# Optimization experiments

Hardware: AMD Instinct MI355X
Metric: run time of the kernel (lower is better)

The kernel has to match this reference:

```python
import jax, jax.numpy as jnp
import numpy as np

H = 256   # node_hidden_dim == edge_hidden_dim

def _ln(x, g, b):
    m = x.mean(-1, keepdims=True)
    v = ((x - m) ** 2).mean(-1, keepdims=True)
    return (x - m) / jnp.sqrt(v + 1e-5) * g + b

def _slnn(x, W, b, g, beta):
    # Linear -> LayerNorm -> ReLU (SingleLayerNN)
    return jax.nn.relu(_ln(x @ W.T + b, g, beta))

def _gru_mean(x, Wih, Whh, bih, bhh):
    # x: [E, T, Din]; torch GRU gate order (r, z, n); returns mean over time of outputs [E, H]
    h0 = jnp.zeros((x.shape[0], Whh.shape[1]), x.dtype)
    def step(h, xt):
        gi = xt @ Wih.T + bih
        gh = h @ Whh.T + bhh
        ir, iz, inn = jnp.split(gi, 3, axis=-1)
        hr, hz, hn = jnp.split(gh, 3, axis=-1)
        r = jax.nn.sigmoid(ir + hr)
        z = jax.nn.sigmoid(iz + hz)
        n = jnp.tanh(inn + r * hn)
        h_new = (1.0 - z) * n + z * h
        return h_new, h_new
    _, ys = jax.lax.scan(step, h0, jnp.swapaxes(x, 0, 1))  # [T, E, H]
    return ys.mean(axis=0)

def setup_inputs() -> dict:
    key = jax.random.key(0)
    ks = iter(jax.random.split(key, 64))
    rn = lambda shape, s=1.0: (jax.random.normal(next(ks), shape, jnp.float32) * s)
    ru = lambda shape: jax.random.uniform(next(ks), shape, jnp.float32)
    ri = lambda shape, hi: jax.random.randint(next(ks), shape, 0, hi, jnp.int32)
    N0, N1, N2, E0, E1, T = 40000, 10000, 2000, 100000, 20000, 8
    Dn, De, FC, C = 128, 64, 512, 16
    inp = {
        'node_features': rn((N0, Dn)),
        'edge_features_0': rn((E0, T, De)),
        'edge_features_1': rn((E1, T, H)),
        'history_0': rn((N0, H)),
        'history_1': rn((N1, H)),
        'agg_history_1': rn((N2, H)),
        'subg_norm_1': ru((N1, 1)),
        'subg_norm_2': ru((N2, 1)),
        'norm_2': ru((N2, 1)),
        'src0': ri((E0,), N0), 'dst0': ri((E0,), N1),
        'src1': ri((E1,), N1), 'dst1': ri((E1,), N2),
        'self_nid0': ri((N1,), N0), 'self_nid1': ri((N2,), N1),
        # parameters
        'gru0_Wih': rn((3 * H, De), 0.05), 'gru0_Whh': rn((3 * H, H), 0.05),
        'gru0_bih': rn((3 * H,), 0.05), 'gru0_bhh': rn((3 * H,), 0.05),
        'gru1_Wih': rn((3 * H, H), 0.05), 'gru1_Whh': rn((3 * H, H), 0.05),
        'gru1_bih': rn((3 * H,), 0.05), 'gru1_bhh': rn((3 * H,), 0.05),
        'phi0_W': rn((H, Dn + H), 0.05), 'phi0_b': rn((H,), 0.05),
        'phi0_g': jnp.ones((H,)), 'phi0_beta': jnp.zeros((H,)),
        'phi1_W': rn((H, 2 * H), 0.05), 'phi1_b': rn((H,), 0.05),
        'phi1_g': jnp.ones((H,)), 'phi1_beta': jnp.zeros((H,)),
        'nu0_W': rn((H, 2 * H), 0.05), 'nu0_b': rn((H,), 0.05),
        'nu0_g': jnp.ones((H,)), 'nu0_beta': jnp.zeros((H,)),
        'nu1_W': rn((H, 2 * H), 0.05), 'nu1_b': rn((H,), 0.05),
        'nu1_g': jnp.ones((H,)), 'nu1_beta': jnp.zeros((H,)),
        'fc1_W': rn((FC, H), 0.05), 'fc1_b': rn((FC,), 0.05),
        'fc2_W': rn((C, FC), 0.05), 'fc2_b': rn((C,), 0.05),
    }
    return inp

def reference(node_features, edge_features_0, edge_features_1, history_0, history_1,
              agg_history_1, subg_norm_1, subg_norm_2, norm_2,
              gru0_Wih, gru0_Whh, gru0_bih, gru0_bhh,
              gru1_Wih, gru1_Whh, gru1_bih, gru1_bhh,
              phi0_W, phi0_b, phi0_g, phi0_beta,
              phi1_W, phi1_b, phi1_g, phi1_beta,
              nu0_W, nu0_b, nu0_g, nu0_beta,
              nu1_W, nu1_b, nu1_g, nu1_beta,
              fc1_W, fc1_b, fc2_W, fc2_b,
              src0, dst0, src1, dst1, self_nid0, self_nid1):
    N1, N2 = self_nid0.shape[0], self_nid1.shape[0]
    # ---- layer 0 ----
    self_h0 = _slnn(jnp.concatenate([jnp.zeros((N1, H), node_features.dtype),
                                     node_features[self_nid0]], 1),
                    phi0_W, phi0_b, phi0_g, phi0_beta)                       # [N1, H]
    edge_emb0 = _gru_mean(edge_features_0, gru0_Wih, gru0_Whh, gru0_bih, gru0_bhh)  # [E0, H]
    nb0 = _slnn(jnp.concatenate([node_features[src0], edge_emb0], 1),
                phi0_W, phi0_b, phi0_g, phi0_beta)
    msg0 = jax.nn.relu(nb0 - history_0[src0])
    delta_nb0 = jax.ops.segment_sum(msg0, dst0, num_segments=N1)             # scatter-sum
    new_h0 = (delta_nb0 - self_h0) * subg_norm_1
    h1 = _slnn(jnp.concatenate([new_h0, self_h0], 1), nu0_W, nu0_b, nu0_g, nu0_beta)  # [N1, H]
    # ---- layer 1 ----
    self_h1 = _slnn(jnp.concatenate([jnp.zeros((N2, H), h1.dtype), h1[self_nid1]], 1),
                    phi1_W, phi1_b, phi1_g, phi1_beta)                       # [N2, H]
    self_delta_h1 = self_h1 - history_1[self_nid1]
    edge_emb1 = _gru_mean(edge_features_1, gru1_Wih, gru1_Whh, gru1_bih, gru1_bhh)  # [E1, H]
    nb1 = _slnn(jnp.concatenate([h1[src1], edge_emb1], 1),
                phi1_W, phi1_b, phi1_g, phi1_beta)
    msg1 = jax.nn.relu(nb1 - history_1[src1])
    delta_nb1 = jax.ops.segment_sum(msg1, dst1, num_segments=N2)
    new_h1 = (delta_nb1 - self_delta_h1) * subg_norm_2 + agg_history_1 * norm_2
    h2 = _slnn(jnp.concatenate([new_h1, self_h1], 1), nu1_W, nu1_b, nu1_g, nu1_beta)  # [N2, H]
    # ---- readout (no activation between fc1 and fc2, as in source) ----
    logit = (h2 @ fc1_W.T + fc1_b) @ fc2_W.T + fc2_b
    return logit
```

## Files before the change

### kernel.cpp

```cpp
#include <hip/hip_runtime.h>

typedef unsigned short u16;
typedef __attribute__((ext_vector_type(4))) float f32x4;
typedef __attribute__((ext_vector_type(8))) short bf16x8;
#define MFMA16(a,b,c) __builtin_amdgcn_mfma_f32_16x16x32_bf16((a),(b),(c),0,0,0)

__device__ __forceinline__ u16 f2bf(float f){
  unsigned int u = __float_as_uint(f);
  u += 0x7FFFu + ((u >> 16) & 1u);
  return (u16)(u >> 16);
}
__device__ __forceinline__ float bf2f(u16 h){
  return __uint_as_float(((unsigned int)h) << 16);
}
__device__ __forceinline__ float sigmoid_f(float x){
  x = fminf(fmaxf(x, -30.f), 30.f);
  return __fdividef(1.f, 1.f + __expf(-x));
}
__device__ __forceinline__ float tanh_f(float x){
  x = fminf(fmaxf(x, -15.f), 15.f);
  float e = __expf(-2.f * x);
  return __fdividef(1.f - e, 1.f + e);
}

__global__ void cvt_bf16_kernel(const float* __restrict__ in, u16* __restrict__ out, int n){
  int i = blockIdx.x * 256 + threadIdx.x;
  int stride = gridDim.x * 256;
  for (; i < n; i += stride) out[i] = f2bf(in[i]);
}

template<int R>
__device__ __forceinline__ void ln_stats_rows(const float* __restrict__ O,
                                              float* __restrict__ mean_s,
                                              float* __restrict__ rstd_s){
  const int tid  = threadIdx.x;
  const int wave = tid >> 6, lane = tid & 63;
  constexpr int RW = R / 4;
  #pragma unroll
  for (int rr = 0; rr < RW; rr++){
    const int r = wave * RW + rr;
    float s = 0.f, q = 0.f;
    #pragma unroll
    for (int i = lane; i < 256; i += 64){ float v = O[r*256 + i]; s += v; q += v*v; }
    #pragma unroll
    for (int off = 32; off; off >>= 1){ s += __shfl_down(s, off); q += __shfl_down(q, off); }
    if (lane == 0){
      float m   = s * (1.f/256.f);
      float var = q * (1.f/256.f) - m*m;
      mean_s[r] = m;
      rstd_s[r] = rsqrtf(fmaxf(var, 0.f) + 1e-5f);
    }
  }
}

template<int DIN, int NFD>
__global__ __launch_bounds__(256, 2)
void gru_mfma_kernel(int E,
    const float* __restrict__ x,
    const float* __restrict__ nodef,
    const int*   __restrict__ src,
    const int*   __restrict__ dst,
    const float* __restrict__ hist,
    const u16*   __restrict__ Wih,
    const u16*   __restrict__ Whh,
    const float* __restrict__ bih,
    const float* __restrict__ bhh,
    const u16*   __restrict__ phiW,
    const float* __restrict__ phib,
    const float* __restrict__ phig,
    const float* __restrict__ phibeta,
    float* __restrict__ delta)
{
  constexpr int HP  = 264;
  constexpr int XW  = (DIN > NFD) ? DIN : NFD;
  constexpr int XLP = XW + 8;
  constexpr int KP  = NFD + 256;

  __shared__ u16  hb[2 * 32 * HP];
  __shared__ u16  xl[32 * XLP];
  __shared__ float sums_s[4 * 32], sqs_s[4 * 32];
  __shared__ float mean_s[32], rstd_s[32];
  __shared__ int   srcs_s[32], dsts_s[32];

  const int tid  = threadIdx.x;
  const int wave = tid >> 6, lane = tid & 63;
  const int quad = lane >> 4, ln15 = lane & 15;
  const int cbase = wave * 64;
  const int e0   = blockIdx.x * 32;

  if (tid < 32){
    int e = e0 + tid;
    int ec = (e < E) ? e : (E - 1);
    srcs_s[tid] = src[ec];
    dsts_s[tid] = dst[ec];
  }

  int cnt[4];
  float brc[4], bzc[4], bnic[4], bnhc[4], pb[4], gg[4], gb[4];
  #pragma unroll
  for (int nt = 0; nt < 4; nt++){
    int c = cbase + nt*16 + ln15;
    cnt[nt]  = c;
    brc[nt]  = bih[c]       + bhh[c];
    bzc[nt]  = bih[256 + c] + bhh[256 + c];
    bnic[nt] = bih[512 + c];
    bnhc[nt] = bhh[512 + c];
    pb[nt]   = phib[c];
    gg[nt]   = phig[c];
    gb[nt]   = phibeta[c];
  }

  const int aoff = ln15 * HP  + quad * 8;
  const int xoff = ln15 * XLP + quad * 8;
  const int qoff = quad * 8;

  float hs[2][4][4];
  #pragma unroll
  for (int mt = 0; mt < 2; mt++)
    #pragma unroll
    for (int nt = 0; nt < 4; nt++)
      #pragma unroll
      for (int q = 0; q < 4; q++) hs[mt][nt][q] = 0.f;

  const f32x4 zero4 = {0.f, 0.f, 0.f, 0.f};

  for (int t = 0; t < 8; t++){
    __syncthreads();
    {
      constexpr int R4 = DIN / 4;
      for (int i = tid; i < 32 * R4; i += 256){
        int e  = i / R4;
        int k4 = (i - e * R4) * 4;
        int ge = (e0 + e < E) ? (e0 + e) : (E - 1);
        const float4 v = *(const float4*)(x + (size_t)ge * (8 * DIN) + (size_t)t * DIN + k4);
        ushort4 u;
        u.x = f2bf(v.x); u.y = f2bf(v.y); u.z = f2bf(v.z); u.w = f2bf(v.w);
        *(ushort4*)(xl + e * XLP + k4) = u;
      }
    }
    __syncthreads();

    const u16* rd = hb + ((t & 1) ^ 1) * (32 * HP);
    u16*       wr = hb + (t & 1) * (32 * HP);

    #pragma unroll 1
    for (int half = 0; half < 2; half++){
      f32x4 aR[2][2], aZ[2][2], aNI[2][2], aNH[2][2];
      #pragma unroll
      for (int mt = 0; mt < 2; mt++)
        #pragma unroll
        for (int j = 0; j < 2; j++){
          aR[mt][j] = zero4; aZ[mt][j] = zero4; aNI[mt][j] = zero4; aNH[mt][j] = zero4;
        }

      if (t > 0){
        #pragma unroll
        for (int kt = 0; kt < 8; kt++){
          bf16x8 a0 = *(const bf16x8*)(rd + aoff + kt * 32);
          bf16x8 a1 = *(const bf16x8*)(rd + aoff + 16 * HP + kt * 32);
          #pragma unroll
          for (int j = 0; j < 2; j++){
            const int nt = half * 2 + j;
            const u16* bp = Whh + (size_t)cnt[nt] * 256 + kt * 32 + qoff;
            bf16x8 br = *(const bf16x8*)(bp);
            bf16x8 bz = *(const bf16x8*)(bp + 256 * 256);
            bf16x8 bn = *(const bf16x8*)(bp + 512 * 256);
            aR[0][j]  = MFMA16(a0, br, aR[0][j]);  aR[1][j]  = MFMA16(a1, br, aR[1][j]);
            aZ[0][j]  = MFMA16(a0, bz, aZ[0][j]);  aZ[1][j]  = MFMA16(a1, bz, aZ[1][j]);
            aNH[0][j] = MFMA16(a0, bn, aNH[0][j]); aNH[1][j] = MFMA16(a1, bn, aNH[1][j]);
          }
        }
      }
      #pragma unroll
      for (int kt = 0; kt < DIN / 32; kt++){
        bf16x8 a0 = *(const bf16x8*)(xl + xoff + kt * 32);
        bf16x8 a1 = *(const bf16x8*)(xl + xoff + 16 * XLP + kt * 32);
        #pragma unroll
        for (int j = 0; j < 2; j++){
          const int nt = half * 2 + j;
          const u16* bp = Wih + (size_t)cnt[nt] * DIN + kt * 32 + qoff;
          bf16x8 br = *(const bf16x8*)(bp);
          bf16x8 bz = *(const bf16x8*)(bp + 256 * DIN);
          bf16x8 bn = *(const bf16x8*)(bp + 512 * DIN);
          aR[0][j]  = MFMA16(a0, br, aR[0][j]);  aR[1][j]  = MFMA16(a1, br, aR[1][j]);
          aZ[0][j]  = MFMA16(a0, bz, aZ[0][j]);  aZ[1][j]  = MFMA16(a1, bz, aZ[1][j]);
          aNI[0][j] = MFMA16(a0, bn, aNI[0][j]); aNI[1][j] = MFMA16(a1, bn, aNI[1][j]);
        }
      }
      #pragma unroll
      for (int mt = 0; mt < 2; mt++)
        #pragma unroll
        for (int j = 0; j < 2; j++){
          const int nt = half * 2 + j;
          const int c  = cnt[nt];
          #pragma unroll
          for (int q = 0; q < 4; q++){
            const int e = mt * 16 + quad * 4 + q;
            float r = sigmoid_f(aR[mt][j][q] + brc[nt]);
            float z = sigmoid_f(aZ[mt][j][q] + bzc[nt]);
            float n = tanh_f(aNI[mt][j][q] + bnic[nt] + r * (aNH[mt][j][q] + bnhc[nt]));
            float hold = (t > 0) ? bf2f(rd[e * HP + c]) : 0.f;
            float hnew = (1.f - z) * n + z * hold;
            hs[mt][nt][q] += hnew;
            if (t < 7) wr[e * HP + c] = f2bf(hnew);
          }
        }
    }
  }

  __syncthreads();
  {
    u16* eb = hb;
    #pragma unroll
    for (int mt = 0; mt < 2; mt++)
      #pragma unroll
      for (int nt = 0; nt < 4; nt++)
        #pragma unroll
        for (int q = 0; q < 4; q++){
          const int e = mt * 16 + quad * 4 + q;
          eb[e * HP + cnt[nt]] = f2bf(hs[mt][nt][q] * 0.125f);
        }
    constexpr int R4 = NFD / 4;
    for (int i = tid; i < 32 * R4; i += 256){
      int e  = i / R4;
      int k4 = (i - e * R4) * 4;
      const float4 v = *(const float4*)(nodef + (size_t)srcs_s[e] * NFD + k4);
      ushort4 u;
      u.x = f2bf(v.x); u.y = f2bf(v.y); u.z = f2bf(v.z); u.w = f2bf(v.w);
      *(ushort4*)(xl + e * XLP + k4) = u;
    }
  }
  __syncthreads();

  f32x4 P[2][4];
  #pragma unroll
  for (int mt = 0; mt < 2; mt++)
    #pragma unroll
    for (int nt = 0; nt < 4; nt++) P[mt][nt] = zero4;

  #pragma unroll
  for (int kt = 0; kt < NFD / 32; kt++){
    bf16x8 a0 = *(const bf16x8*)(xl + xoff + kt * 32);
    bf16x8 a1 = *(const bf16x8*)(xl + xoff + 16 * XLP + kt * 32);
    #pragma unroll
    for (int nt = 0; nt < 4; nt++){
      const u16* bp = phiW + (size_t)cnt[nt] * KP + kt * 32 + qoff;
      bf16x8 b = *(const bf16x8*)(bp);
      P[0][nt] = MFMA16(a0, b, P[0][nt]);
      P[1][nt] = MFMA16(a1, b, P[1][nt]);
    }
  }
  #pragma unroll
  for (int kt = 0; kt < 8; kt++){
    bf16x8 a0 = *(const bf16x8*)(hb + aoff + kt * 32);
    bf16x8 a1 = *(const bf16x8*)(hb + aoff + 16 * HP + kt * 32);
    #pragma unroll
    for (int nt = 0; nt < 4; nt++){
      const u16* bp = phiW + (size_t)cnt[nt] * KP + NFD + kt * 32 + qoff;
      bf16x8 b = *(const bf16x8*)(bp);
      P[0][nt] = MFMA16(a0, b, P[0][nt]);
      P[1][nt] = MFMA16(a1, b, P[1][nt]);
    }
  }

  float sl[2][4], sq[2][4];
  #pragma unroll
  for (int mt = 0; mt < 2; mt++)
    #pragma unroll
    for (int q = 0; q < 4; q++){ sl[mt][q] = 0.f; sq[mt][q] = 0.f; }
  #pragma unroll
  for (int mt = 0; mt < 2; mt++)
    #pragma unroll
    for (int nt = 0; nt < 4; nt++)
      #pragma unroll
      for (int q = 0; q < 4; q++){
        float v = P[mt][nt][q] + pb[nt];
        P[mt][nt][q] = v;
        sl[mt][q] += v;
        sq[mt][q] += v * v;
      }
  #pragma unroll
  for (int off = 1; off < 16; off <<= 1){
    #pragma unroll
    for (int mt = 0; mt < 2; mt++)
      #pragma unroll
      for (int q = 0; q < 4; q++){
        sl[mt][q] += __shfl_xor(sl[mt][q], off);
        sq[mt][q] += __shfl_xor(sq[mt][q], off);
      }
  }
  if (ln15 == 0){
    #pragma unroll
    for (int mt = 0; mt < 2; mt++)
      #pragma unroll
      for (int q = 0; q < 4; q++){
        int row = mt * 16 + quad * 4 + q;
        sums_s[wave * 32 + row] = sl[mt][q];
        sqs_s[wave * 32 + row]  = sq[mt][q];
      }
  }
  __syncthreads();
  if (tid < 32){
    float m = 0.f, qq = 0.f;
    #pragma unroll
    for (int w = 0; w < 4; w++){ m += sums_s[w * 32 + tid]; qq += sqs_s[w * 32 + tid]; }
    m  *= (1.f / 256.f);
    qq *= (1.f / 256.f);
    mean_s[tid] = m;
    rstd_s[tid] = rsqrtf(fmaxf(qq - m * m, 0.f) + 1e-5f);
  }
  __syncthreads();

  #pragma unroll
  for (int mt = 0; mt < 2; mt++)
    #pragma unroll
    for (int nt = 0; nt < 4; nt++){
      const int c = cnt[nt];
      #pragma unroll
      for (int q = 0; q < 4; q++){
        const int e  = mt * 16 + quad * 4 + q;
        const int ge = e0 + e;
        float y = (P[mt][nt][q] - mean_s[e]) * rstd_s[e] * gg[nt] + gb[nt];
        y = fmaxf(y, 0.f);
        float mv = y - hist[(size_t)srcs_s[e] * 256 + c];
        if (ge < E && mv > 0.f)
          atomicAdd(delta + (size_t)dsts_s[e] * 256 + c, mv);
      }
    }
}

template<int K, int WS>
__global__ __launch_bounds__(256)
void self_slnn_kernel(int N,
    const float* __restrict__ feat,
    const int*   __restrict__ nid,
    const float* __restrict__ W,
    const float* __restrict__ b,
    const float* __restrict__ g,
    const float* __restrict__ beta,
    const float* __restrict__ hist,
    float* __restrict__ out,
    float* __restrict__ out2)
{
  constexpr int R = 8;
  __shared__ float X[R*K];
  __shared__ float O[R*256];
  __shared__ float mean_s[R], rstd_s[R];
  __shared__ int   nids[R];
  const int tid = threadIdx.x;
  const int n0  = blockIdx.x * R;
  if (tid < R) nids[tid] = (n0 + tid < N) ? nid[n0 + tid] : 0;
  __syncthreads();
  for (int i = tid; i < R*K; i += 256){
    int r = i / K, k = i - r*K;
    X[i] = feat[(size_t)nids[r]*K + k];
  }
  __syncthreads();
  const int c = tid;
  const float* Wc = W + (size_t)c*WS + (WS - K);
  float acc[R];
  const float bc0 = b[c];
  #pragma unroll
  for (int r = 0; r < R; r++) acc[r] = bc0;
  #pragma unroll 1
  for (int k = 0; k < K; k += 4){
    float4 w = *(const float4*)(Wc + k);
    #pragma unroll
    for (int r = 0; r < R; r++){
      float4 xv = *(const float4*)(X + r*K + k);
      acc[r] += w.x*xv.x + w.y*xv.y + w.z*xv.z + w.w*xv.w;
    }
  }
  #pragma unroll
  for (int r = 0; r < R; r++) O[r*256 + c] = acc[r];
  __syncthreads();
  ln_stats_rows<R>(O, mean_s, rstd_s);
  __syncthreads();
  const float gc = g[c], bc = beta[c];
  #pragma unroll
  for (int r = 0; r < R; r++){
    int n = n0 + r;
    if (n < N){
      float y = fmaxf((acc[r] - mean_s[r]) * rstd_s[r] * gc + bc, 0.f);
      out[(size_t)n*256 + c] = y;
      if (out2) out2[(size_t)n*256 + c] = y - hist[(size_t)nids[r]*256 + c];
    }
  }
}

__global__ __launch_bounds__(256)
void compose_slnn_kernel(int N,
    const float* __restrict__ delta,
    const float* __restrict__ selfA,
    const float* __restrict__ selfB,
    const float* __restrict__ subg,
    const float* __restrict__ agg,
    const float* __restrict__ normv,
    const float* __restrict__ W,
    const float* __restrict__ b,
    const float* __restrict__ g,
    const float* __restrict__ beta,
    float* __restrict__ out)
{
  constexpr int R = 8;
  __shared__ float X[R*512];
  __shared__ float O[R*256];
  __shared__ float mean_s[R], rstd_s[R];
  const int tid = threadIdx.x;
  const int n0  = blockIdx.x * R;
  for (int i = tid; i < R*512; i += 256){
    int r = i >> 9, k = i & 511;
    int n = n0 + r;
    float v = 0.f;
    if (n < N){
      if (k < 256){
        v = (delta[(size_t)n*256 + k] - selfA[(size_t)n*256 + k]) * subg[n];
        if (agg) v += agg[(size_t)n*256 + k] * normv[n];
      } else {
        v = selfB[(size_t)n*256 + (k - 256)];
      }
    }
    X[i] = v;
  }
  __syncthreads();
  const int c = tid;
  const float* Wc = W + (size_t)c*512;
  float acc[R];
  const float bc0 = b[c];
  #pragma unroll
  for (int r = 0; r < R; r++) acc[r] = bc0;
  #pragma unroll 1
  for (int k = 0; k < 512; k += 4){
    float4 w = *(const float4*)(Wc + k);
    #pragma unroll
    for (int r = 0; r < R; r++){
      float4 xv = *(const float4*)(X + r*512 + k);
      acc[r] += w.x*xv.x + w.y*xv.y + w.z*xv.z + w.w*xv.w;
    }
  }
  #pragma unroll
  for (int r = 0; r < R; r++) O[r*256 + c] = acc[r];
  __syncthreads();
  ln_stats_rows<R>(O, mean_s, rstd_s);
  __syncthreads();
  const float gc = g[c], bc = beta[c];
  #pragma unroll
  for (int r = 0; r < R; r++){
    int n = n0 + r;
    if (n < N)
      out[(size_t)n*256 + c] = fmaxf((acc[r] - mean_s[r]) * rstd_s[r] * gc + bc, 0.f);
  }
}

__global__ __launch_bounds__(256)
void readout_kernel(int N,
    const float* __restrict__ h2,
    const float* __restrict__ W1,
    const float* __restrict__ b1,
    const float* __restrict__ W2,
    const float* __restrict__ b2,
    float* __restrict__ out)
{
  constexpr int R = 8;
  __shared__ float X[R*256];
  __shared__ float T[R*512];
  const int tid = threadIdx.x;
  const int n0  = blockIdx.x * R;
  for (int i = tid; i < R*256; i += 256){
    int r = i >> 8, k = i & 255;
    int n = n0 + r;
    X[i] = (n < N) ? h2[(size_t)n*256 + k] : 0.f;
  }
  __syncthreads();
  const int c = tid;
  const float* Wa = W1 + (size_t)c*256;
  const float* Wb = W1 + (size_t)(c+256)*256;
  float acca[R], accb[R];
  const float ba = b1[c], bb = b1[c+256];
  #pragma unroll
  for (int r = 0; r < R; r++){ acca[r] = ba; accb[r] = bb; }
  #pragma unroll 1
  for (int k = 0; k < 256; k += 4){
    float4 wa = *(const float4*)(Wa + k);
    float4 wb = *(const float4*)(Wb + k);
    #pragma unroll
    for (int r = 0; r < R; r++){
      float4 xv = *(const float4*)(X + r*256 + k);
      acca[r] += wa.x*xv.x + wa.y*xv.y + wa.z*xv.z + wa.w*xv.w;
      accb[r] += wb.x*xv.x + wb.y*xv.y + wb.z*xv.z + wb.w*xv.w;
    }
  }
  #pragma unroll
  for (int r = 0; r < R; r++){ T[r*512 + c] = acca[r]; T[r*512 + 256 + c] = accb[r]; }
  __syncthreads();
  if (tid < R*16){
    int r = tid >> 4, o = tid & 15;
    int n = n0 + r;
    if (n < N){
      float s = b2[o];
      const float* w  = W2 + (size_t)o*512;
      const float* tr = T + r*512;
      #pragma unroll 4
      for (int k = 0; k < 512; k++) s += tr[k]*w[k];
      out[(size_t)n*16 + o] = s;
    }
  }
}

extern "C" void kernel_launch(void* const* d_in, const int* in_sizes, int n_in,
                              void* d_out, int out_size, void* d_ws, size_t ws_size,
                              hipStream_t stream) {
  const float* nf     = (const float*)d_in[0];
  const float* x0     = (const float*)d_in[1];
  const float* x1     = (const float*)d_in[2];
  const float* hist0  = (const float*)d_in[3];
  const float* hist1  = (const float*)d_in[4];
  const float* aggh1  = (const float*)d_in[5];
  const float* subg1  = (const float*)d_in[6];
  const float* subg2  = (const float*)d_in[7];
  const float* norm2  = (const float*)d_in[8];
  const int*   src0   = (const int*)d_in[9];
  const int*   dst0   = (const int*)d_in[10];
  const int*   src1   = (const int*)d_in[11];
  const int*   dst1   = (const int*)d_in[12];
  const int*   nid0   = (const int*)d_in[13];
  const int*   nid1   = (const int*)d_in[14];
  const float* g0Wih  = (const float*)d_in[15];
  const float* g0Whh  = (const float*)d_in[16];
  const float* g0bih  = (const float*)d_in[17];
  const float* g0bhh  = (const float*)d_in[18];
  const float* g1Wih  = (const float*)d_in[19];
  const float* g1Whh  = (const float*)d_in[20];
  const float* g1bih  = (const float*)d_in[21];
  const float* g1bhh  = (const float*)d_in[22];
  const float* phi0W  = (const float*)d_in[23];
  const float* phi0b  = (const float*)d_in[24];
  const float* phi0g  = (const float*)d_in[25];
  const float* phi0be = (const float*)d_in[26];
  const float* phi1W  = (const float*)d_in[27];
  const float* phi1b  = (const float*)d_in[28];
  const float* phi1g  = (const float*)d_in[29];
  const float* phi1be = (const float*)d_in[30];
  const float* nu0W   = (const float*)d_in[31];
  const float* nu0b   = (const float*)d_in[32];
  const float* nu0g   = (const float*)d_in[33];
  const float* nu0be  = (const float*)d_in[34];
  const float* nu1W   = (const float*)d_in[35];
  const float* nu1b   = (const float*)d_in[36];
  const float* nu1g   = (const float*)d_in[37];
  const float* nu1be  = (const float*)d_in[38];
  const float* fc1W   = (const float*)d_in[39];
  const float* fc1b   = (const float*)d_in[40];
  const float* fc2W   = (const float*)d_in[41];
  const float* fc2b   = (const float*)d_in[42];

  const int E0 = in_sizes[9];
  const int E1 = in_sizes[11];
  const int N1 = in_sizes[13];
  const int N2 = in_sizes[14];

  float* ws     = (float*)d_ws;
  float* delta0 = ws;
  float* selfh0 = delta0 + (size_t)N1*256;
  float* h1p    = selfh0 + (size_t)N1*256;
  float* delta1 = h1p    + (size_t)N1*256;
  float* selfh1 = delta1 + (size_t)N2*256;
  float* selfd1 = selfh1 + (size_t)N2*256;
  float* h2p    = selfd1 + (size_t)N2*256;

  u16* wbf       = (u16*)(h2p + (size_t)N2*256);
  u16* g0Wih_bf  = wbf;
  u16* g0Whh_bf  = g0Wih_bf + 768*64;
  u16* phi0W_bf  = g0Whh_bf + 768*256;
  u16* g1Wih_bf  = phi0W_bf + 256*384;
  u16* g1Whh_bf  = g1Wih_bf + 768*256;
  u16* phi1W_bf  = g1Whh_bf + 768*256;

  hipMemsetAsync(delta0, 0, (size_t)N1*256*sizeof(float), stream);
  hipMemsetAsync(delta1, 0, (size_t)N2*256*sizeof(float), stream);

  cvt_bf16_kernel<<<192, 256, 0, stream>>>(g0Wih, g0Wih_bf, 768*64);
  cvt_bf16_kernel<<<768, 256, 0, stream>>>(g0Whh, g0Whh_bf, 768*256);
  cvt_bf16_kernel<<<384, 256, 0, stream>>>(phi0W, phi0W_bf, 256*384);
  cvt_bf16_kernel<<<768, 256, 0, stream>>>(g1Wih, g1Wih_bf, 768*256);
  cvt_bf16_kernel<<<768, 256, 0, stream>>>(g1Whh, g1Whh_bf, 768*256);
  cvt_bf16_kernel<<<512, 256, 0, stream>>>(phi1W, phi1W_bf, 256*512);

  const int gN1 = (N1 + 7) / 8;
  const int gN2 = (N2 + 7) / 8;

  self_slnn_kernel<128, 384><<<gN1, 256, 0, stream>>>(
      N1, nf, nid0, phi0W, phi0b, phi0g, phi0be, nullptr, selfh0, nullptr);

  gru_mfma_kernel<64, 128><<<(E0 + 31) / 32, 256, 0, stream>>>(
      E0, x0, nf, src0, dst0, hist0,
      g0Wih_bf, g0Whh_bf, g0bih, g0bhh,
      phi0W_bf, phi0b, phi0g, phi0be, delta0);

  compose_slnn_kernel<<<gN1, 256, 0, stream>>>(
      N1, delta0, selfh0, selfh0, subg1, nullptr, nullptr,
      nu0W, nu0b, nu0g, nu0be, h1p);

  self_slnn_kernel<256, 512><<<gN2, 256, 0, stream>>>(
      N2, h1p, nid1, phi1W, phi1b, phi1g, phi1be, hist1, selfh1, selfd1);

  gru_mfma_kernel<256, 256><<<(E1 + 31) / 32, 256, 0, stream>>>(
      E1, x1, h1p, src1, dst1, hist1,
      g1Wih_bf, g1Whh_bf, g1bih, g1bhh,
      phi1W_bf, phi1b, phi1g, phi1be, delta1);

  compose_slnn_kernel<<<gN2, 256, 0, stream>>>(
      N2, delta1, selfd1, selfh1, subg2, aggh1, norm2,
      nu1W, nu1b, nu1g, nu1be, h2p);

  readout_kernel<<<gN2, 256, 0, stream>>>(
      N2, h2p, fc1W, fc1b, fc2W, fc2b, (float*)d_out);

  (void)n_in; (void)out_size; (void)ws_size;
}
```

Baseline: 3.263 ms.

## Restructure GRU MFMA kernel with larger edge tiles, chunked LDS layout, register prefetch

Rewrites the fused GRU+phi kernel to take a templated edge tile (64 for layer 0), so each Whh/Wih fragment loaded from global feeds more MFMAs. Shared memory moves to a k-chunk-major layout without padding, the previous hidden state stays packed in registers, and the next timestep's input is prefetched into registers during compute. It also folds biases into the accumulator init, uses faster exp2/rcp sigmoid/tanh without clamping, and uses packed bf16 conversion. In exchange, register pressure and LDS use rise, which may cut occupancy, and the approximate activations can change accuracy slightly.

```diff
diff --git a/kernel.cpp b/kernel.cpp
--- a/kernel.cpp
+++ b/kernel.cpp
@@ -13,6 +13,30 @@
 __device__ __forceinline__ float bf2f(u16 h){
   return __uint_as_float(((unsigned int)h) << 16);
 }
+
+#if defined(__has_builtin)
+#  if __has_builtin(__builtin_amdgcn_cvt_pk_bf16_f32)
+#    define PK_BF16 1
+#  endif
+#endif
+__device__ __forceinline__ unsigned int pack_bf(float a, float b){
+#ifdef PK_BF16
+  auto v = __builtin_amdgcn_cvt_pk_bf16_f32(a, b);
+  return __builtin_bit_cast(unsigned int, v);
+#else
+  return (unsigned int)f2bf(a) | ((unsigned int)f2bf(b) << 16);
+#endif
+}
+
+__device__ __forceinline__ float fsig(float x){
+  float e = __builtin_amdgcn_exp2f(-1.44269504f * x);
+  return __builtin_amdgcn_rcpf(1.f + e);
+}
+__device__ __forceinline__ float ftanh(float x){
+  float e = __builtin_amdgcn_exp2f(2.88539008f * x);
+  return 1.f - 2.f * __builtin_amdgcn_rcpf(1.f + e);
+}
+
 __device__ __forceinline__ float sigmoid_f(float x){
   x = fminf(fmaxf(x, -30.f), 30.f);
   return __fdividef(1.f, 1.f + __expf(-x));
@@ -53,9 +77,9 @@
   }
 }
 
-template<int DIN, int NFD>
+template<int TM, int DIN, int NFD>
 __global__ __launch_bounds__(256, 2)
-void gru_mfma_kernel(int E,
+void gru_mfma2_kernel(int E,
     const float* __restrict__ x,
     const float* __restrict__ nodef,
     const int*   __restrict__ src,
@@ -71,218 +95,249 @@
     const float* __restrict__ phibeta,
     float* __restrict__ delta)
 {
-  constexpr int HP  = 264;
-  constexpr int XW  = (DIN > NFD) ? DIN : NFD;
-  constexpr int XLP = XW + 8;
-  constexpr int KP  = NFD + 256;
-
-  __shared__ u16  hb[2 * 32 * HP];
-  __shared__ u16  xl[32 * XLP];
-  __shared__ float sums_s[4 * 32], sqs_s[4 * 32];
-  __shared__ float mean_s[32], rstd_s[32];
-  __shared__ int   srcs_s[32], dsts_s[32];
+  constexpr int MT = TM / 16;
+  constexpr int KP = NFD + 256;
+  constexpr int HB = TM * 256;
+
+  __shared__ u16  hb[2 * HB];
+  __shared__ u16  xl[TM * DIN];
+  __shared__ float sums_s[4 * TM], sqs_s[4 * TM];
+  __shared__ float mean_s[TM], rstd_s[TM];
+  __shared__ int   srcs_s[TM], dsts_s[TM];
 
   const int tid  = threadIdx.x;
   const int wave = tid >> 6, lane = tid & 63;
   const int quad = lane >> 4, ln15 = lane & 15;
   const int cbase = wave * 64;
-  const int e0   = blockIdx.x * 32;
-
-  if (tid < 32){
+  const int e0   = blockIdx.x * TM;
+
+  if (tid < TM){
     int e = e0 + tid;
     int ec = (e < E) ? e : (E - 1);
     srcs_s[tid] = src[ec];
     dsts_s[tid] = dst[ec];
   }
 
-  int cnt[4];
-  float brc[4], bzc[4], bnic[4], bnhc[4], pb[4], gg[4], gb[4];
+  float brc[4], bzc[4], bnic[4], bnhc[4];
   #pragma unroll
   for (int nt = 0; nt < 4; nt++){
-    int c = cbase + nt*16 + ln15;
-    cnt[nt]  = c;
+    int c = cbase + nt * 16 + ln15;
     brc[nt]  = bih[c]       + bhh[c];
     bzc[nt]  = bih[256 + c] + bhh[256 + c];
     bnic[nt] = bih[512 + c];
     bnhc[nt] = bhh[512 + c];
-    pb[nt]   = phib[c];
-    gg[nt]   = phig[c];
-    gb[nt]   = phibeta[c];
-  }
-
-  const int aoff = ln15 * HP  + quad * 8;
-  const int xoff = ln15 * XLP + quad * 8;
+  }
+
   const int qoff = quad * 8;
 
-  float hs[2][4][4];
-  #pragma unroll
-  for (int mt = 0; mt < 2; mt++)
-    #pragma unroll
-    for (int nt = 0; nt < 4; nt++)
-      #pragma unroll
-      for (int q = 0; q < 4; q++) hs[mt][nt][q] = 0.f;
-
-  const f32x4 zero4 = {0.f, 0.f, 0.f, 0.f};
-
+  constexpr int TPR = 256 / TM;
+  constexpr int CPT = DIN / TPR;
+  const int srow   = tid / TPR;
+  const int schunk = (tid - srow * TPR) * CPT;
+  const float* xrowp = x + (size_t)((e0 + srow < E) ? (e0 + srow) : (E - 1)) * (8 * DIN) + schunk;
+
+  float4 xr[CPT / 4];
+  #pragma unroll
+  for (int i = 0; i < CPT / 4; i++) xr[i] = *(const float4*)(xrowp + i * 4);
+
+  f32x4 hs[4][MT];
+  unsigned int hprev[4][MT][2];
+  #pragma unroll
+  for (int nt = 0; nt < 4; nt++)
+    #pragma unroll
+    for (int mt = 0; mt < MT; mt++){
+      hs[nt][mt] = (f32x4){0.f,0.f,0.f,0.f};
+      hprev[nt][mt][0] = 0u; hprev[nt][mt][1] = 0u;
+    }
+
+  #pragma unroll 1
   for (int t = 0; t < 8; t++){
     __syncthreads();
-    {
-      constexpr int R4 = DIN / 4;
-      for (int i = tid; i < 32 * R4; i += 256){
-        int e  = i / R4;
-        int k4 = (i - e * R4) * 4;
-        int ge = (e0 + e < E) ? (e0 + e) : (E - 1);
-        const float4 v = *(const float4*)(x + (size_t)ge * (8 * DIN) + (size_t)t * DIN + k4);
-        ushort4 u;
-        u.x = f2bf(v.x); u.y = f2bf(v.y); u.z = f2bf(v.z); u.w = f2bf(v.w);
-        *(ushort4*)(xl + e * XLP + k4) = u;
-      }
+    #pragma unroll
+    for (int i = 0; i < CPT / 8; i++){
+      uint4 w;
+      w.x = pack_bf(xr[2*i].x,   xr[2*i].y);
+      w.y = pack_bf(xr[2*i].z,   xr[2*i].w);
+      w.z = pack_bf(xr[2*i+1].x, xr[2*i+1].y);
+      w.w = pack_bf(xr[2*i+1].z, xr[2*i+1].w);
+      *(uint4*)(xl + ((schunk/8 + i) * TM + srow) * 8) = w;
     }
     __syncthreads();
 
-    const u16* rd = hb + ((t & 1) ^ 1) * (32 * HP);
-    u16*       wr = hb + (t & 1) * (32 * HP);
-
-    #pragma unroll 1
-    for (int half = 0; half < 2; half++){
-      f32x4 aR[2][2], aZ[2][2], aNI[2][2], aNH[2][2];
-      #pragma unroll
-      for (int mt = 0; mt < 2; mt++)
-        #pragma unroll
-        for (int j = 0; j < 2; j++){
-          aR[mt][j] = zero4; aZ[mt][j] = zero4; aNI[mt][j] = zero4; aNH[mt][j] = zero4;
-        }
+    const u16* rd = hb + ((t + 1) & 1) * HB;
+    u16*       wr = hb + (t & 1) * HB;
+
+    #pragma unroll
+    for (int nt = 0; nt < 4; nt++){
+      const int c = cbase + nt * 16 + ln15;
+      f32x4 aR  = {brc[nt],  brc[nt],  brc[nt],  brc[nt]};
+      f32x4 aZ  = {bzc[nt],  bzc[nt],  bzc[nt],  bzc[nt]};
+      f32x4 aNI = {bnic[nt], bnic[nt], bnic[nt], bnic[nt]};
+      f32x4 aNH = {bnhc[nt], bnhc[nt], bnhc[nt], bnhc[nt]};
+      f32x4 accR[MT], accZ[MT], accNI[MT], accNH[MT];
+      #pragma unroll
+      for (int mt = 0; mt < MT; mt++){ accR[mt]=aR; accZ[mt]=aZ; accNI[mt]=aNI; accNH[mt]=aNH; }
 
       if (t > 0){
         #pragma unroll
         for (int kt = 0; kt < 8; kt++){
-          bf16x8 a0 = *(const bf16x8*)(rd + aoff + kt * 32);
-          bf16x8 a1 = *(const bf16x8*)(rd + aoff + 16 * HP + kt * 32);
+          bf16x8 a[MT];
           #pragma unroll
-          for (int j = 0; j < 2; j++){
-            const int nt = half * 2 + j;
-            const u16* bp = Whh + (size_t)cnt[nt] * 256 + kt * 32 + qoff;
-            bf16x8 br = *(const bf16x8*)(bp);
-            bf16x8 bz = *(const bf16x8*)(bp + 256 * 256);
-            bf16x8 bn = *(const bf16x8*)(bp + 512 * 256);
-            aR[0][j]  = MFMA16(a0, br, aR[0][j]);  aR[1][j]  = MFMA16(a1, br, aR[1][j]);
-            aZ[0][j]  = MFMA16(a0, bz, aZ[0][j]);  aZ[1][j]  = MFMA16(a1, bz, aZ[1][j]);
-            aNH[0][j] = MFMA16(a0, bn, aNH[0][j]); aNH[1][j] = MFMA16(a1, bn, aNH[1][j]);
+          for (int mt = 0; mt < MT; mt++)
+            a[mt] = *(const bf16x8*)(rd + ((kt*4 + quad) * TM + mt*16 + ln15) * 8);
+          const u16* bp = Whh + (size_t)c * 256 + kt * 32 + qoff;
+          bf16x8 br = *(const bf16x8*)(bp);
+          bf16x8 bz = *(const bf16x8*)(bp + 256 * 256);
+          bf16x8 bn = *(const bf16x8*)(bp + 512 * 256);
+          #pragma unroll
+          for (int mt = 0; mt < MT; mt++){
+            accR[mt]  = MFMA16(a[mt], br, accR[mt]);
+            accZ[mt]  = MFMA16(a[mt], bz, accZ[mt]);
+            accNH[mt] = MFMA16(a[mt], bn, accNH[mt]);
           }
         }
       }
       #pragma unroll
       for (int kt = 0; kt < DIN / 32; kt++){
-        bf16x8 a0 = *(const bf16x8*)(xl + xoff + kt * 32);
-        bf16x8 a1 = *(const bf16x8*)(xl + xoff + 16 * XLP + kt * 32);
+        bf16x8 a[MT];
         #pragma unroll
-        for (int j = 0; j < 2; j++){
-          const int nt = half * 2 + j;
-          const u16* bp = Wih + (size_t)cnt[nt] * DIN + kt * 32 + qoff;
-          bf16x8 br = *(const bf16x8*)(bp);
-          bf16x8 bz = *(const bf16x8*)(bp + 256 * DIN);
-          bf16x8 bn = *(const bf16x8*)(bp + 512 * DIN);
-          aR[0][j]  = MFMA16(a0, br, aR[0][j]);  aR[1][j]  = MFMA16(a1, br, aR[1][j]);
-          aZ[0][j]  = MFMA16(a0, bz, aZ[0][j]);  aZ[1][j]  = MFMA16(a1, bz, aZ[1][j]);
-          aNI[0][j] = MFMA16(a0, bn, aNI[0][j]); aNI[1][j] = MFMA16(a1, bn, aNI[1][j]);
+        for (int mt = 0; mt < MT; mt++)
+          a[mt] = *(const bf16x8*)(xl + ((kt*4 + quad) * TM + mt*16 + ln15) * 8);
+        const u16* up = Wih + (size_t)c * DIN + kt * 32 + qoff;
+        bf16x8 ur = *(const bf16x8*)(up);
+        bf16x8 uz = *(const bf16x8*)(up + 256 * DIN);
+        bf16x8 un = *(const bf16x8*)(up + 512 * DIN);
+        #pragma unroll
+        for (int mt = 0; mt < MT; mt++){
+          accR[mt]  = MFMA16(a[mt], ur, accR[mt]);
+          accZ[mt]  = MFMA16(a[mt], uz, accZ[mt]);
+          accNI[mt] = MFMA16(a[mt], un, accNI[mt]);
         }
       }
-      #pragma unroll
-      for (int mt = 0; mt < 2; mt++)
+
+      #pragma unroll
+      for (int mt = 0; mt < MT; mt++){
+        const int wbase = ((c >> 3) * TM + mt*16 + quad*4) * 8 + (c & 7);
         #pragma unroll
-        for (int j = 0; j < 2; j++){
-          const int nt = half * 2 + j;
-          const int c  = cnt[nt];
-          #pragma unroll
-          for (int q = 0; q < 4; q++){
-            const int e = mt * 16 + quad * 4 + q;
-            float r = sigmoid_f(aR[mt][j][q] + brc[nt]);
-            float z = sigmoid_f(aZ[mt][j][q] + bzc[nt]);
-            float n = tanh_f(aNI[mt][j][q] + bnic[nt] + r * (aNH[mt][j][q] + bnhc[nt]));
-            float hold = (t > 0) ? bf2f(rd[e * HP + c]) : 0.f;
-            float hnew = (1.f - z) * n + z * hold;
-            hs[mt][nt][q] += hnew;
-            if (t < 7) wr[e * HP + c] = f2bf(hnew);
+        for (int p = 0; p < 2; p++){
+          float h0 = bf2f((u16)(hprev[nt][mt][p]));
+          float h1 = bf2f((u16)(hprev[nt][mt][p] >> 16));
+          float r0 = fsig(accR[mt][2*p]),   r1 = fsig(accR[mt][2*p+1]);
+          float z0 = fsig(accZ[mt][2*p]),   z1 = fsig(accZ[mt][2*p+1]);
+          float n0 = ftanh(accNI[mt][2*p]   + r0 * accNH[mt][2*p]);
+          float n1 = ftanh(accNI[mt][2*p+1] + r1 * accNH[mt][2*p+1]);
+          float hn0 = n0 + z0 * (h0 - n0);
+          float hn1 = n1 + z1 * (h1 - n1);
+          hs[nt][mt][2*p]   += hn0;
+          hs[nt][mt][2*p+1] += hn1;
+          unsigned int pk = pack_bf(hn0, hn1);
+          hprev[nt][mt][p] = pk;
+          if (t < 7){
+            wr[wbase + (2*p)   * 8] = (u16)pk;
+            wr[wbase + (2*p+1) * 8] = (u16)(pk >> 16);
           }
         }
-    }
-  }
-
-  __syncthreads();
+      }
+      asm volatile("" ::: "memory");
+    }
+
+    if (t < 7){
+      const float* xp = xrowp + (t + 1) * DIN;
+      #pragma unroll
+      for (int i = 0; i < CPT / 4; i++) xr[i] = *(const float4*)(xp + i * 4);
+    }
+  }
+
+  __syncthreads();
+
   {
     u16* eb = hb;
     #pragma unroll
-    for (int mt = 0; mt < 2; mt++)
-      #pragma unroll
-      for (int nt = 0; nt < 4; nt++)
+    for (int nt = 0; nt < 4; nt++){
+      const int c = cbase + nt * 16 + ln15;
+      #pragma unroll
+      for (int mt = 0; mt < MT; mt++){
+        const int base = ((c >> 3) * TM + mt*16 + quad*4) * 8 + (c & 7);
         #pragma unroll
-        for (int q = 0; q < 4; q++){
-          const int e = mt * 16 + quad * 4 + q;
-          eb[e * HP + cnt[nt]] = f2bf(hs[mt][nt][q] * 0.125f);
-        }
-    constexpr int R4 = NFD / 4;
-    for (int i = tid; i < 32 * R4; i += 256){
-      int e  = i / R4;
-      int k4 = (i - e * R4) * 4;
-      const float4 v = *(const float4*)(nodef + (size_t)srcs_s[e] * NFD + k4);
-      ushort4 u;
-      u.x = f2bf(v.x); u.y = f2bf(v.y); u.z = f2bf(v.z); u.w = f2bf(v.w);
-      *(ushort4*)(xl + e * XLP + k4) = u;
-    }
-  }
-  __syncthreads();
-
-  f32x4 P[2][4];
-  #pragma unroll
-  for (int mt = 0; mt < 2; mt++)
-    #pragma unroll
-    for (int nt = 0; nt < 4; nt++) P[mt][nt] = zero4;
-
-  #pragma unroll
-  for (int kt = 0; kt < NFD / 32; kt++){
-    bf16x8 a0 = *(const bf16x8*)(xl + xoff + kt * 32);
-    bf16x8 a1 = *(const bf16x8*)(xl + xoff + 16 * XLP + kt * 32);
-    #pragma unroll
-    for (int nt = 0; nt < 4; nt++){
-      const u16* bp = phiW + (size_t)cnt[nt] * KP + kt * 32 + qoff;
-      bf16x8 b = *(const bf16x8*)(bp);
-      P[0][nt] = MFMA16(a0, b, P[0][nt]);
-      P[1][nt] = MFMA16(a1, b, P[1][nt]);
-    }
-  }
-  #pragma unroll
-  for (int kt = 0; kt < 8; kt++){
-    bf16x8 a0 = *(const bf16x8*)(hb + aoff + kt * 32);
-    bf16x8 a1 = *(const bf16x8*)(hb + aoff + 16 * HP + kt * 32);
-    #pragma unroll
-    for (int nt = 0; nt < 4; nt++){
-      const u16* bp = phiW + (size_t)cnt[nt] * KP + NFD + kt * 32 + qoff;
-      bf16x8 b = *(const bf16x8*)(bp);
-      P[0][nt] = MFMA16(a0, b, P[0][nt]);
-      P[1][nt] = MFMA16(a1, b, P[1][nt]);
-    }
-  }
-
-  float sl[2][4], sq[2][4];
-  #pragma unroll
-  for (int mt = 0; mt < 2; mt++)
+        for (int q = 0; q < 4; q++)
+          eb[base + q * 8] = f2bf(hs[nt][mt][q] * 0.125f);
+      }
+    }
+    u16* nb = hb + HB;
+    constexpr int NCPT = NFD / TPR;
+    const int nrow   = tid / TPR;
+    const int nchunk = (tid - nrow * TPR) * NCPT;
+    const float* np = nodef + (size_t)srcs_s[nrow] * NFD + nchunk;
+    #pragma unroll
+    for (int i = 0; i < NCPT / 8; i++){
+      float4 va = *(const float4*)(np + i * 8);
+      float4 vb = *(const float4*)(np + i * 8 + 4);
+      uint4 w;
+      w.x = pack_bf(va.x, va.y); w.y = pack_bf(va.z, va.w);
+      w.z = pack_bf(vb.x, vb.y); w.w = pack_bf(vb.z, vb.w);
+      *(uint4*)(nb + ((nchunk/8 + i) * TM + nrow) * 8) = w;
+    }
+  }
+  __syncthreads();
+
+  float pb[4], gg[4], gb[4];
+  #pragma unroll
+  for (int nt = 0; nt < 4; nt++){
+    int c = cbase + nt * 16 + ln15;
+    pb[nt] = phib[c]; gg[nt] = phig[c]; gb[nt] = phibeta[c];
+  }
+
+  f32x4 P[4][MT];
+  #pragma unroll
+  for (int nt = 0; nt < 4; nt++)
+    #pragma unroll
+    for (int mt = 0; mt < MT; mt++)
+      P[nt][mt] = (f32x4){pb[nt], pb[nt], pb[nt], pb[nt]};
+
+  #pragma unroll
+  for (int nt = 0; nt < 4; nt++){
+    const int c = cbase + nt * 16 + ln15;
+    #pragma unroll
+    for (int kt = 0; kt < NFD / 32; kt++){
+      bf16x8 a[MT];
+      #pragma unroll
+      for (int mt = 0; mt < MT; mt++)
+        a[mt] = *(const bf16x8*)(hb + HB + ((kt*4 + quad) * TM + mt*16 + ln15) * 8);
+      bf16x8 b = *(const bf16x8*)(phiW + (size_t)c * KP + kt * 32 + qoff);
+      #pragma unroll
+      for (int mt = 0; mt < MT; mt++) P[nt][mt] = MFMA16(a[mt], b, P[nt][mt]);
+    }
+    #pragma unroll
+    for (int kt = 0; kt < 8; kt++){
+      bf16x8 a[MT];
+      #pragma unroll
+      for (int mt = 0; mt < MT; mt++)
+        a[mt] = *(const bf16x8*)(hb + ((kt*4 + quad) * TM + mt*16 + ln15) * 8);
+      bf16x8 b = *(const bf16x8*)(phiW + (size_t)c * KP + NFD + kt * 32 + qoff);
+      #pragma unroll
+      for (int mt = 0; mt < MT; mt++) P[nt][mt] = MFMA16(a[mt], b, P[nt][mt]);
+    }
+    asm volatile("" ::: "memory");
+  }
+
+  float sl[MT][4], sq[MT][4];
+  #pragma unroll
+  for (int mt = 0; mt < MT; mt++)
     #pragma unroll
     for (int q = 0; q < 4; q++){ sl[mt][q] = 0.f; sq[mt][q] = 0.f; }
   #pragma unroll
-  for (int mt = 0; mt < 2; mt++)
-    #pragma unroll
-    for (int nt = 0; nt < 4; nt++)
+  for (int nt = 0; nt < 4; nt++)
+    #pragma unroll
+    for (int mt = 0; mt < MT; mt++)
       #pragma unroll
       for (int q = 0; q < 4; q++){
-        float v = P[mt][nt][q] + pb[nt];
-        P[mt][nt][q] = v;
-        sl[mt][q] += v;
-        sq[mt][q] += v * v;
+        float v = P[nt][mt][q];
+        sl[mt][q] += v; sq[mt][q] += v * v;
       }
   #pragma unroll
   for (int off = 1; off < 16; off <<= 1){
     #pragma unroll
-    for (int mt = 0; mt < 2; mt++)
+    for (int mt = 0; mt < MT; mt++)
       #pragma unroll
       for (int q = 0; q < 4; q++){
         sl[mt][q] += __shfl_xor(sl[mt][q], off);
@@ -291,19 +346,19 @@
   }
   if (ln15 == 0){
     #pragma unroll
-    for (int mt = 0; mt < 2; mt++)
+    for (int mt = 0; mt < MT; mt++)
       #pragma unroll
       for (int q = 0; q < 4; q++){
-        int row = mt * 16 + quad * 4 + q;
-        sums_s[wave * 32 + row] = sl[mt][q];
-        sqs_s[wave * 32 + row]  = sq[mt][q];
-      }
-  }
-  __syncthreads();
-  if (tid < 32){
+        int row = mt*16 + quad*4 + q;
+        sums_s[wave * TM + row] = sl[mt][q];
+        sqs_s[wave * TM + row]  = sq[mt][q];
+      }
+  }
+  __syncthreads();
+  if (tid < TM){
     float m = 0.f, qq = 0.f;
     #pragma unroll
-    for (int w = 0; w < 4; w++){ m += sums_s[w * 32 + tid]; qq += sqs_s[w * 32 + tid]; }
+    for (int w = 0; w < 4; w++){ m += sums_s[w * TM + tid]; qq += sqs_s[w * TM + tid]; }
     m  *= (1.f / 256.f);
     qq *= (1.f / 256.f);
     mean_s[tid] = m;
@@ -312,21 +367,22 @@
   __syncthreads();
 
   #pragma unroll
-  for (int mt = 0; mt < 2; mt++)
-    #pragma unroll
-    for (int nt = 0; nt < 4; nt++){
-      const int c = cnt[nt];
+  for (int nt = 0; nt < 4; nt++){
+    const int c = cbase + nt * 16 + ln15;
+    #pragma unroll
+    for (int mt = 0; mt < MT; mt++){
       #pragma unroll
       for (int q = 0; q < 4; q++){
-        const int e  = mt * 16 + quad * 4 + q;
+        const int e  = mt*16 + quad*4 + q;
         const int ge = e0 + e;
-        float y = (P[mt][nt][q] - mean_s[e]) * rstd_s[e] * gg[nt] + gb[nt];
+        float y = (P[nt][mt][q] - mean_s[e]) * rstd_s[e] * gg[nt] + gb[nt];
         y = fmaxf(y, 0.f);
         float mv = y - hist[(size_t)srcs_s[e] * 256 + c];
         if (ge < E && mv > 0.f)
           atomicAdd(delta + (size_t)dsts_s[e] * 256 + c, mv);
       }
     }
+  }
 }
 
 template<int K, int WS>
@@ -592,7 +648,7 @@
   self_slnn_kernel<128, 384><<<gN1, 256, 0, stream>>>(
       N1, nf, nid0, phi0W, phi0b, phi0g, phi0be, nullptr, selfh0, nullptr);
 
-  gru_mfma_kernel<64, 128><<<(E0 + 31) / 32, 256, 0, stream>>>(
+  gru_mfma2_kernel<64, 64, 128><<<(E0 + 63) / 64, 256, 0, stream>>>(
       E0, x0, nf, src0, dst0, hist0,
       g0Wih_bf, g0Whh_bf, g0bih, g0bhh,
       phi0W_bf, phi0b, phi0g, phi0be, delta0);
@@ -604,7 +660,7 @@
   self_slnn_kernel<256, 512><<<gN2, 256, 0, stream>>>(
       N2, h1p, nid1, phi1W, phi1b, phi1g, phi1be, hist1, selfh1, selfd1);
 
-  gru_mfma_kernel<256, 256><<<(E1 + 31) / 32, 256, 0, stream>>>(
+  gru_mfma2_kernel<32, 256, 256><<<(E1 + 31) / 32, 256, 0, stream>>>(
       E1, x1, h1p, src1, dst1, hist1,
       g1Wih_bf, g1Whh_bf, g1bih, g1bhh,
       phi1W_bf, phi1b, phi1g, phi1be, delta1);
```

New measurement: 3.545 ms. 8.7% more time.
